# Kernel optimization log

Hardware: AMD Instinct MI355X
Metric: run time of the kernel (lower is better)

The kernel has to match this reference:

```python
import jax, jax.numpy as jnp
import numpy as np

B, S, DM, H = 4, 1024, 1024, 16
D = DM // H  # head size 64


def setup_inputs() -> dict:
    key = jax.random.key(0)
    ks = jax.random.split(key, 8)
    scale = 1.0 / np.sqrt(DM)
    return {
        "hidden_states": jax.random.normal(ks[0], (B, S, DM), dtype=jnp.float32),
        "attention_mask": jnp.zeros((B, 1, 1, S), dtype=jnp.float32),
        "link_mask": jax.random.uniform(ks[1], (B, 1, S, S), dtype=jnp.float32),
        "Wq": jax.random.normal(ks[2], (DM, DM), dtype=jnp.float32) * scale,
        "bq": jnp.zeros((DM,), dtype=jnp.float32),
        "Wk": jax.random.normal(ks[3], (DM, DM), dtype=jnp.float32) * scale,
        "bk": jnp.zeros((DM,), dtype=jnp.float32),
        "Wv": jax.random.normal(ks[4], (DM, DM), dtype=jnp.float32) * scale,
        "bv": jnp.zeros((DM,), dtype=jnp.float32),
    }


def _split_heads(x):
    # [B,S,DM] -> [B,H,S,D]
    return x.reshape(B, S, H, D).transpose(0, 2, 1, 3)


def reference(hidden_states, attention_mask, link_mask, Wq, bq, Wk, bk, Wv, bv):
    q = _split_heads(hidden_states @ Wq.T + bq)
    k = _split_heads(hidden_states @ Wk.T + bk)
    v = _split_heads(hidden_states @ Wv.T + bv)
    # [B,H,S,S]
    scores = jnp.einsum("bhqd,bhkd->bhqk", q, k) / jnp.float32(np.sqrt(D))
    scores = scores + attention_mask  # additive mask, broadcast [B,1,1,S]
    probs = jax.nn.softmax(scores, axis=-1)
    # post-softmax multiplicative link mask (un-normalizes rows)
    probs = probs * link_mask
    # dropout prob 0.0 (eval) -> identity
    ctx = jnp.einsum("bhqk,bhkd->bhqd", probs, v)
    ctx = ctx.transpose(0, 2, 1, 3).reshape(B, S, DM)
    return ctx
```

## Files before the change

kernel.cpp:

```cpp
#include <hip/hip_runtime.h>
#include <hip/hip_bf16.h>
#include <cstdint>

typedef __attribute__((ext_vector_type(8))) __bf16 bf16x8;
typedef __attribute__((ext_vector_type(4))) float f32x4;
typedef unsigned short u16;
typedef unsigned int u32;

struct alignas(8) U16x4 { u16 x, y, z, w; };
struct alignas(8) U32x2 { u32 x, y; };

__device__ __forceinline__ u16 f2b(float x) {
    u32 u = __builtin_bit_cast(u32, x);
    u += 0x7fffu + ((u >> 16) & 1u);
    return (u16)(u >> 16);
}
__device__ __forceinline__ u32 cvtpk(float lo, float hi) {
    u32 r;
    asm("v_cvt_pk_bf16_f32 %0, %1, %2" : "=v"(r) : "v"(lo), "v"(hi));
    return r;
}

__global__ __launch_bounds__(256) void cvt_kernel(
    const float* __restrict__ hs,
    const float* __restrict__ wq, const float* __restrict__ wk, const float* __restrict__ wv,
    u16* __restrict__ hsb, u16* __restrict__ wb)
{
    int i = blockIdx.x * 256 + threadIdx.x;
    const float4* src; u16* dst; int off;
    if (i < 1048576) { src = (const float4*)hs; dst = hsb; off = i; }
    else {
        int j = i - 1048576;
        int w = j >> 18;
        int o = j & 262143;
        src = (const float4*)(w == 0 ? wq : (w == 1 ? wk : wv));
        dst = wb + w * 1048576;
        off = o;
    }
    float4 v = src[off];
    U16x4 r; r.x = f2b(v.x); r.y = f2b(v.y); r.z = f2b(v.z); r.w = f2b(v.w);
    *(U16x4*)(dst + off * 4) = r;
}

__global__ __launch_bounds__(256, 3) void qkv_gemm(
    const u16* __restrict__ A, const u16* __restrict__ W,
    const float* __restrict__ bq, const float* __restrict__ bk, const float* __restrict__ bv,
    u16* __restrict__ Qo, u16* __restrict__ Ko, u16* __restrict__ Vt)
{
    __shared__ u16 As[2][128 * 32];
    __shared__ u16 Bs[2][128 * 32];
    const int tid = threadIdx.x;
    const int lane = tid & 63, wid = tid >> 6;
    const int wr = (wid >> 1) * 64, wc = (wid & 1) * 64;
    const int g = lane >> 4, c = lane & 15;

    int lin = blockIdx.y * 24 + blockIdx.x;
    int wg = (lin & 7) * 96 + (lin >> 3);
    const int bn = wg >> 5;
    const int bm = wg & 31;

    f32x4 acc[4][4] = {};

#define GSTAGE(bf, k0)                                                              \
    {                                                                               \
        _Pragma("unroll") for (int i = 0; i < 2; ++i) {                             \
            int chunk = i * 256 + tid;                                              \
            int row = chunk >> 2, col = (chunk & 3) * 8;                            \
            const u16* ga = A + (bm * 128 + row) * 1024 + (k0) + col;               \
            const u16* gb = W + (bn * 128 + row) * 1024 + (k0) + col;               \
            u16* la = &As[bf][0] + (i * 256 + wid * 64) * 8;                        \
            u16* lb = &Bs[bf][0] + (i * 256 + wid * 64) * 8;                        \
            __builtin_amdgcn_global_load_lds((const __attribute__((address_space(1))) u32*)ga, \
                                             (__attribute__((address_space(3))) u32*)la, 16, 0, 0); \
            __builtin_amdgcn_global_load_lds((const __attribute__((address_space(1))) u32*)gb, \
                                             (__attribute__((address_space(3))) u32*)lb, 16, 0, 0); \
        }                                                                           \
    }

    GSTAGE(0, 0);
    __syncthreads();

    int cur = 0;
    for (int t = 0; t < 32; ++t) {
        if (t < 31) GSTAGE(cur ^ 1, (t + 1) * 32);
        bf16x8 af[4], bf4[4];
        #pragma unroll
        for (int i = 0; i < 4; ++i)
            af[i] = *(const bf16x8*)(&As[cur][0] + (wr + i * 16 + c) * 32 + g * 8);
        #pragma unroll
        for (int j = 0; j < 4; ++j)
            bf4[j] = *(const bf16x8*)(&Bs[cur][0] + (wc + j * 16 + c) * 32 + g * 8);
        #pragma unroll
        for (int i = 0; i < 4; ++i)
            #pragma unroll
            for (int j = 0; j < 4; ++j)
                acc[i][j] = __builtin_amdgcn_mfma_f32_16x16x32_bf16(af[i], bf4[j], acc[i][j], 0, 0, 0);
        __syncthreads();
        cur ^= 1;
    }
#undef GSTAGE

    const int region = bn >> 3;
    const float* bias = region == 0 ? bq : (region == 1 ? bk : bv);
    #pragma unroll
    for (int i = 0; i < 4; ++i) {
        int m0 = bm * 128 + wr + i * 16 + g * 4;
        int b = m0 >> 10, s0 = m0 & 1023;
        #pragma unroll
        for (int j = 0; j < 4; ++j) {
            int n = (bn & 7) * 128 + wc + j * 16 + c;
            float bb = bias[n];
            int h = n >> 6, d = n & 63;
            int bh = b * 16 + h;
            if (region == 2) {
                U16x4 pk;
                pk.x = f2b(acc[i][j][0] + bb);
                pk.y = f2b(acc[i][j][1] + bb);
                pk.z = f2b(acc[i][j][2] + bb);
                pk.w = f2b(acc[i][j][3] + bb);
                *(U16x4*)(Vt + (bh * 64 + d) * 1024 + s0) = pk;
            } else if (region == 1) {
                #pragma unroll
                for (int r = 0; r < 4; ++r)
                    Ko[(bh * 1024 + s0 + r) * 64 + d] = f2b(acc[i][j][r] + bb);
            } else {
                #pragma unroll
                for (int r = 0; r < 4; ++r)
                    Qo[(bh * 1024 + s0 + r) * 64 + d] = f2b((acc[i][j][r] + bb) * 0.125f);
            }
        }
    }
}

__global__ __launch_bounds__(256, 4) void attn_kernel(
    const u16* __restrict__ Q, const u16* __restrict__ K, const u16* __restrict__ Vt,
    const float* __restrict__ amask, const float* __restrict__ link,
    float* __restrict__ out)
{
    __shared__ u16 Ks[2][64 * 64];
    __shared__ u16 Vs[2][64 * 64];
    __shared__ u16 P[4][16 * 64];
    const int tid = threadIdx.x;
    const int lane = tid & 63, wid = tid >> 6;
    const int g = lane >> 4, c = lane & 15;
    const int c7 = c & 7;

    int hw = blockIdx.x;
    int logical = (hw & 7) * 128 + (hw >> 3);
    int b = logical >> 8;
    int qt = (logical >> 4) & 15;
    int h = logical & 15;
    int bh = b * 16 + h;
    const int qbase = qt * 64 + wid * 16;

    const u16* Qh = Q + bh * 65536;
    const u16* Kh = K + bh * 65536;
    const u16* Vh = Vt + bh * 65536;
    const float* mk = amask + b * 1024;
    const float* lkq = link + (size_t)b * 1048576 + (size_t)(qbase + c) * 1024;

    bf16x8 qfx0 = *(const bf16x8*)(Qh + (qbase + c) * 64 + g * 8);
    bf16x8 qfx1 = *(const bf16x8*)(Qh + (qbase + c) * 64 + 32 + g * 8);

    float lsum = 0.f;
    f32x4 ctx[4] = {};
    u16* const Pb = &P[wid][0];

#define ASTAGE(bf, kv)                                                              \
    {                                                                               \
        _Pragma("unroll") for (int i = 0; i < 2; ++i) {                             \
            int chunk = i * 256 + tid;                                              \
            int row = chunk >> 3;                                                   \
            int scir = (chunk & 7) ^ (row & 7);                                     \
            const u16* gk = Kh + ((kv) + row) * 64 + scir * 8;                      \
            const u16* gv = Vh + row * 1024 + (kv) + scir * 8;                      \
            u16* lk = &Ks[bf][0] + (i * 256 + wid * 64) * 8;                        \
            u16* lv = &Vs[bf][0] + (i * 256 + wid * 64) * 8;                        \
            __builtin_amdgcn_global_load_lds((const __attribute__((address_space(1))) u32*)gk, \
                                             (__attribute__((address_space(3))) u32*)lk, 16, 0, 0); \
            __builtin_amdgcn_global_load_lds((const __attribute__((address_space(1))) u32*)gv, \
                                             (__attribute__((address_space(3))) u32*)lv, 16, 0, 0); \
        }                                                                           \
    }

    ASTAGE(0, 0);
    __syncthreads();

    int cur = 0;
    for (int t = 0; t < 16; ++t) {
        if (t < 15) ASTAGE(cur ^ 1, (t + 1) * 64);
        const int kv = t * 64;
        const u16* Kb = &Ks[cur][0];
        const u16* Vb = &Vs[cur][0];

        f32x4 m4[4], lk4[4];
        #pragma unroll
        for (int kt = 0; kt < 4; ++kt) {
            m4[kt]  = *(const f32x4*)(mk  + kv + kt * 16 + g * 4);
            lk4[kt] = *(const f32x4*)(lkq + kv + kt * 16 + g * 4);
        }

        #pragma unroll
        for (int kt = 0; kt < 4; ++kt) {
            bf16x8 kf0 = *(const bf16x8*)(Kb + (kt * 16 + c) * 64 + ((g)     ^ c7) * 8);
            bf16x8 kf1 = *(const bf16x8*)(Kb + (kt * 16 + c) * 64 + ((4 + g) ^ c7) * 8);
            f32x4 sc = {};
            sc = __builtin_amdgcn_mfma_f32_16x16x32_bf16(kf0, qfx0, sc, 0, 0, 0);
            sc = __builtin_amdgcn_mfma_f32_16x16x32_bf16(kf1, qfx1, sc, 0, 0, 0);
            float e0 = __expf(sc[0] + m4[kt][0]);
            float e1 = __expf(sc[1] + m4[kt][1]);
            float e2 = __expf(sc[2] + m4[kt][2]);
            float e3 = __expf(sc[3] + m4[kt][3]);
            lsum += (e0 + e1) + (e2 + e3);
            U32x2 pw;
            pw.x = cvtpk(e0 * lk4[kt][0], e1 * lk4[kt][1]);
            pw.y = cvtpk(e2 * lk4[kt][2], e3 * lk4[kt][3]);
            *(U32x2*)(Pb + c * 64 + (((kt * 4 + g) ^ (c7 << 1)) * 4)) = pw;
        }
        __builtin_amdgcn_s_setprio(1);
        #pragma unroll
        for (int kk = 0; kk < 2; ++kk) {
            bf16x8 pf = *(const bf16x8*)(Pb + c * 64 + (((kk * 8 + g * 2) ^ (c7 << 1)) * 4));
            #pragma unroll
            for (int dt = 0; dt < 4; ++dt) {
                bf16x8 vf = *(const bf16x8*)(Vb + (dt * 16 + c) * 64 + ((kk * 4 + g) ^ c7) * 8);
                ctx[dt] = __builtin_amdgcn_mfma_f32_16x16x32_bf16(pf, vf, ctx[dt], 0, 0, 0);
            }
        }
        __builtin_amdgcn_s_setprio(0);
        __syncthreads();
        cur ^= 1;
    }
#undef ASTAGE

    lsum += __shfl_xor(lsum, 16, 64);
    lsum += __shfl_xor(lsum, 32, 64);

    #pragma unroll
    for (int r = 0; r < 4; ++r) {
        float inv = 1.0f / __shfl(lsum, g * 4 + r, 16);
        int q = qbase + g * 4 + r;
        float* orow = out + (size_t)b * 1048576 + (size_t)q * 1024 + h * 64;
        #pragma unroll
        for (int dt = 0; dt < 4; ++dt)
            orow[dt * 16 + c] = ctx[dt][r] * inv;
    }
}

extern "C" void kernel_launch(void* const* d_in, const int* in_sizes, int n_in,
                              void* d_out, int out_size, void* d_ws, size_t ws_size,
                              hipStream_t stream)
{
    (void)in_sizes; (void)n_in; (void)out_size; (void)ws_size;
    const float* hs    = (const float*)d_in[0];
    const float* amask = (const float*)d_in[1];
    const float* link  = (const float*)d_in[2];
    const float* Wq    = (const float*)d_in[3];
    const float* bq    = (const float*)d_in[4];
    const float* Wk    = (const float*)d_in[5];
    const float* bk    = (const float*)d_in[6];
    const float* Wv    = (const float*)d_in[7];
    const float* bv    = (const float*)d_in[8];
    float* out = (float*)d_out;

    char* ws = (char*)d_ws;
    u16* hsb = (u16*)ws;
    u16* wb  = (u16*)(ws + (8u  << 20));
    u16* Qb  = (u16*)(ws + (14u << 20));
    u16* Kb  = (u16*)(ws + (22u << 20));
    u16* Vtb = (u16*)(ws + (30u << 20));

    cvt_kernel<<<7168, 256, 0, stream>>>(hs, Wq, Wk, Wv, hsb, wb);
    qkv_gemm<<<dim3(24, 32), 256, 0, stream>>>(hsb, wb, bq, bk, bv, Qb, Kb, Vtb);
    attn_kernel<<<1024, 256, 0, stream>>>(Qb, Kb, Vtb, amask, link, out);
}
```

Measured before the change: 97.67 us.

## Split attention KV range across two wave groups per block with LDS reduction

The attention block grows to 512 threads: two groups of four waves each process half of the key range (32-key tiles) for the same 64 queries, and their partial context and row sums are combined through shared memory at the end. K is staged asynchronously into LDS while V is loaded into registers and stored to LDS after a barrier. The aim is to raise waves in flight to hide latency of the link-mask reads and the MFMA chains. In exchange it adds a second barrier per iteration, smaller per-iteration MFMA work, and an epilogue reduction through shared memory.

Result: slower. 115.4 us (+18.2%).

```diff
diff --git a/kernel.cpp b/kernel.cpp
--- a/kernel.cpp
+++ b/kernel.cpp
@@ -132,18 +132,22 @@
     }
 }
 
-__global__ __launch_bounds__(256, 4) void attn_kernel(
+__global__ __launch_bounds__(512, 8) void attn_kernel(
     const u16* __restrict__ Q, const u16* __restrict__ K, const u16* __restrict__ Vt,
     const float* __restrict__ amask, const float* __restrict__ link,
     float* __restrict__ out)
 {
-    __shared__ u16 Ks[2][64 * 64];
-    __shared__ u16 Vs[2][64 * 64];
-    __shared__ u16 P[4][16 * 64];
+    __shared__ u16 Ks[2][2][32 * 64];
+    __shared__ u16 Vs[2][64 * 32];
+    __shared__ u16 P[8][16 * 32];
     const int tid = threadIdx.x;
     const int lane = tid & 63, wid = tid >> 6;
     const int g = lane >> 4, c = lane & 15;
     const int c7 = c & 7;
+    const int u2 = (c & 3) ^ ((c >> 2) & 3);
+
+    const int half = wid >> 2;
+    const int qs   = wid & 3;
 
     int hw = blockIdx.x;
     int logical = (hw & 7) * 128 + (hw >> 3);
@@ -151,7 +155,7 @@
     int qt = (logical >> 4) & 15;
     int h = logical & 15;
     int bh = b * 16 + h;
-    const int qbase = qt * 64 + wid * 16;
+    const int qbase = qt * 64 + qs * 16;
 
     const u16* Qh = Q + bh * 65536;
     const u16* Kh = K + bh * 65536;
@@ -162,88 +166,103 @@
     bf16x8 qfx0 = *(const bf16x8*)(Qh + (qbase + c) * 64 + g * 8);
     bf16x8 qfx1 = *(const bf16x8*)(Qh + (qbase + c) * 64 + 32 + g * 8);
 
+    const int sHalf = tid >> 8;
+    const int sIdx  = tid & 255;
+    const int kRow = sIdx >> 3, kCir = sIdx & 7;
+    const u16* KhS = Kh + (sHalf * 512 + kRow) * 64 + ((kCir ^ (kRow & 7)) * 8);
+    u16* const kDst = &Ks[sHalf][0][0] + sIdx * 8;
+    const int vRow = sIdx >> 2, vCir = sIdx & 3;
+    const int vSlot = vCir ^ ((vRow & 3) ^ ((vRow >> 2) & 3));
+    const u16* VhS = Vh + vRow * 1024 + sHalf * 512 + vCir * 8;
+    u16* const vDst = &Vs[sHalf][0] + (vRow * 4 + vSlot) * 8;
+
+#define KSTAGE(buf, kvt)                                                            \
+    __builtin_amdgcn_global_load_lds(                                               \
+        (const __attribute__((address_space(1))) u32*)(KhS + (kvt) * 64),           \
+        (__attribute__((address_space(3))) u32*)(kDst + (buf) * 2048), 16, 0, 0);
+
     float lsum = 0.f;
     f32x4 ctx[4] = {};
     u16* const Pb = &P[wid][0];
-
-#define ASTAGE(bf, kv)                                                              \
-    {                                                                               \
-        _Pragma("unroll") for (int i = 0; i < 2; ++i) {                             \
-            int chunk = i * 256 + tid;                                              \
-            int row = chunk >> 3;                                                   \
-            int scir = (chunk & 7) ^ (row & 7);                                     \
-            const u16* gk = Kh + ((kv) + row) * 64 + scir * 8;                      \
-            const u16* gv = Vh + row * 1024 + (kv) + scir * 8;                      \
-            u16* lk = &Ks[bf][0] + (i * 256 + wid * 64) * 8;                        \
-            u16* lv = &Vs[bf][0] + (i * 256 + wid * 64) * 8;                        \
-            __builtin_amdgcn_global_load_lds((const __attribute__((address_space(1))) u32*)gk, \
-                                             (__attribute__((address_space(3))) u32*)lk, 16, 0, 0); \
-            __builtin_amdgcn_global_load_lds((const __attribute__((address_space(1))) u32*)gv, \
-                                             (__attribute__((address_space(3))) u32*)lv, 16, 0, 0); \
-        }                                                                           \
-    }
-
-    ASTAGE(0, 0);
-    __syncthreads();
-
-    int cur = 0;
+    const u16* const KbBase = &Ks[half][0][0];
+    const u16* const Vb = &Vs[half][0];
+
+    {
+        uint4 v0 = *(const uint4*)(VhS);
+        KSTAGE(0, 0);
+        __syncthreads();
+        *(uint4*)vDst = v0;
+        __syncthreads();
+    }
+
     for (int t = 0; t < 16; ++t) {
-        if (t < 15) ASTAGE(cur ^ 1, (t + 1) * 64);
-        const int kv = t * 64;
-        const u16* Kb = &Ks[cur][0];
-        const u16* Vb = &Vs[cur][0];
-
-        f32x4 m4[4], lk4[4];
-        #pragma unroll
-        for (int kt = 0; kt < 4; ++kt) {
-            m4[kt]  = *(const f32x4*)(mk  + kv + kt * 16 + g * 4);
-            lk4[kt] = *(const f32x4*)(lkq + kv + kt * 16 + g * 4);
-        }
-
-        #pragma unroll
-        for (int kt = 0; kt < 4; ++kt) {
+        uint4 vn = {};
+        if (t < 15) {
+            vn = *(const uint4*)(VhS + (t + 1) * 32);
+            KSTAGE((t + 1) & 1, (t + 1) * 32);
+        }
+        const int kv = half * 512 + t * 32;
+        const u16* Kb = KbBase + (t & 1) * 2048;
+
+        #pragma unroll
+        for (int kt = 0; kt < 2; ++kt) {
+            f32x4 m4  = *(const f32x4*)(mk  + kv + kt * 16 + g * 4);
+            f32x4 lk4 = *(const f32x4*)(lkq + kv + kt * 16 + g * 4);
             bf16x8 kf0 = *(const bf16x8*)(Kb + (kt * 16 + c) * 64 + ((g)     ^ c7) * 8);
             bf16x8 kf1 = *(const bf16x8*)(Kb + (kt * 16 + c) * 64 + ((4 + g) ^ c7) * 8);
             f32x4 sc = {};
             sc = __builtin_amdgcn_mfma_f32_16x16x32_bf16(kf0, qfx0, sc, 0, 0, 0);
             sc = __builtin_amdgcn_mfma_f32_16x16x32_bf16(kf1, qfx1, sc, 0, 0, 0);
-            float e0 = __expf(sc[0] + m4[kt][0]);
-            float e1 = __expf(sc[1] + m4[kt][1]);
-            float e2 = __expf(sc[2] + m4[kt][2]);
-            float e3 = __expf(sc[3] + m4[kt][3]);
+            float e0 = __expf(sc[0] + m4[0]);
+            float e1 = __expf(sc[1] + m4[1]);
+            float e2 = __expf(sc[2] + m4[2]);
+            float e3 = __expf(sc[3] + m4[3]);
             lsum += (e0 + e1) + (e2 + e3);
             U32x2 pw;
-            pw.x = cvtpk(e0 * lk4[kt][0], e1 * lk4[kt][1]);
-            pw.y = cvtpk(e2 * lk4[kt][2], e3 * lk4[kt][3]);
-            *(U32x2*)(Pb + c * 64 + (((kt * 4 + g) ^ (c7 << 1)) * 4)) = pw;
+            pw.x = cvtpk(e0 * lk4[0], e1 * lk4[1]);
+            pw.y = cvtpk(e2 * lk4[2], e3 * lk4[3]);
+            *(U32x2*)(Pb + c * 32 + (((kt * 4 + g) ^ (u2 << 1)) * 4)) = pw;
         }
         __builtin_amdgcn_s_setprio(1);
-        #pragma unroll
-        for (int kk = 0; kk < 2; ++kk) {
-            bf16x8 pf = *(const bf16x8*)(Pb + c * 64 + (((kk * 8 + g * 2) ^ (c7 << 1)) * 4));
-            #pragma unroll
-            for (int dt = 0; dt < 4; ++dt) {
-                bf16x8 vf = *(const bf16x8*)(Vb + (dt * 16 + c) * 64 + ((kk * 4 + g) ^ c7) * 8);
-                ctx[dt] = __builtin_amdgcn_mfma_f32_16x16x32_bf16(pf, vf, ctx[dt], 0, 0, 0);
-            }
+        bf16x8 pf = *(const bf16x8*)(Pb + c * 32 + (((g * 2) ^ (u2 << 1)) * 4));
+        #pragma unroll
+        for (int dt = 0; dt < 4; ++dt) {
+            bf16x8 vf = *(const bf16x8*)(Vb + ((dt * 16 + c) * 4 + (g ^ u2)) * 8);
+            ctx[dt] = __builtin_amdgcn_mfma_f32_16x16x32_bf16(pf, vf, ctx[dt], 0, 0, 0);
         }
         __builtin_amdgcn_s_setprio(0);
         __syncthreads();
-        cur ^= 1;
-    }
-#undef ASTAGE
+        if (t < 15) *(uint4*)vDst = vn;
+        __syncthreads();
+    }
+#undef KSTAGE
 
     lsum += __shfl_xor(lsum, 16, 64);
     lsum += __shfl_xor(lsum, 32, 64);
 
-    #pragma unroll
-    for (int r = 0; r < 4; ++r) {
-        float inv = 1.0f / __shfl(lsum, g * 4 + r, 16);
-        int q = qbase + g * 4 + r;
-        float* orow = out + (size_t)b * 1048576 + (size_t)q * 1024 + h * 64;
+    float* Mc = (float*)&Ks[0][0][0];
+    float* Ml = (float*)&P[0][0];
+    if (half == 1) {
         #pragma unroll
         for (int dt = 0; dt < 4; ++dt)
-            orow[dt * 16 + c] = ctx[dt][r] * inv;
+            #pragma unroll
+            for (int r = 0; r < 4; ++r)
+                Mc[qs * 1024 + (g * 4 + r) * 64 + dt * 16 + c] = ctx[dt][r];
+        if (g == 0) Ml[qs * 16 + c] = lsum;
+    }
+    __syncthreads();
+    if (half == 0) {
+        float lT = lsum + Ml[qs * 16 + c];
+        #pragma unroll
+        for (int r = 0; r < 4; ++r) {
+            float inv = 1.0f / __shfl(lT, g * 4 + r, 16);
+            int q = qbase + g * 4 + r;
+            float* orow = out + (size_t)b * 1048576 + (size_t)q * 1024 + h * 64;
+            #pragma unroll
+            for (int dt = 0; dt < 4; ++dt)
+                orow[dt * 16 + c] =
+                    (ctx[dt][r] + Mc[qs * 1024 + (g * 4 + r) * 64 + dt * 16 + c]) * inv;
+        }
     }
 }
 
@@ -272,5 +291,5 @@
 
     cvt_kernel<<<7168, 256, 0, stream>>>(hs, Wq, Wk, Wv, hsb, wb);
     qkv_gemm<<<dim3(24, 32), 256, 0, stream>>>(hsb, wb, bq, bk, bv, Qb, Kb, Vtb);
-    attn_kernel<<<1024, 256, 0, stream>>>(Qb, Kb, Vtb, amask, link, out);
-}
+    attn_kernel<<<1024, 512, 0, stream>>>(Qb, Kb, Vtb, amask, link, out);
+}
```
